# Kernel tuning notes

Measured on AMD Instinct MI355X. Metric: run time of the kernel, lower is better.

Reference implementation:

```python
import jax, jax.numpy as jnp
import numpy as np
from jax import lax

IMAGE_SIZE = 1280
STRIDE = 32
FMP = IMAGE_SIZE // STRIDE          # 40
BPC = 5                             # boxes per cell (5 anchors)
NUM_CLASSES = 80
NMS_THRESH = 0.5
CONF_THRESH = 0.3
N_BOX = FMP * FMP * BPC             # 8000 candidates
ANCHOR_SIZE = np.array([[17, 25], [55, 75], [92, 206], [202, 21], [289, 311]], dtype=np.float32)


def _make_anchors():
    # generate_anchors: per-cell (x,y) grid repeated for each of BPC anchors, tiled anchor wh
    ys, xs = jnp.meshgrid(jnp.arange(FMP, dtype=jnp.float32), jnp.arange(FMP, dtype=jnp.float32), indexing='ij')
    xy = jnp.stack([xs, ys], axis=-1).reshape(-1, 1, 2)                       # [HW,1,2]
    anchor_xy = jnp.broadcast_to(xy, (FMP * FMP, BPC, 2)).reshape(-1, 2)      # [N,2]
    anchor_wh = jnp.broadcast_to(jnp.asarray(ANCHOR_SIZE)[None], (FMP * FMP, BPC, 2)).reshape(-1, 2)
    return jnp.concatenate([anchor_xy, anchor_wh], axis=-1)                   # [N,4]


def setup_inputs() -> dict:
    key = jax.random.key(0)
    k = jax.random.split(key, 5)
    return {
        'cls_feat': jax.random.normal(k[0], (1, 512, FMP, FMP), jnp.float32),
        'reg_feat': jax.random.normal(k[1], (1, 512, FMP, FMP), jnp.float32),
        'w_obj': jax.random.normal(k[2], (BPC, 512), jnp.float32) * 0.02,
        'b_obj': jnp.zeros((BPC,), jnp.float32),
        'w_cls': jax.random.normal(k[3], (NUM_CLASSES * BPC, 512), jnp.float32) * 0.02,
        'b_cls': jnp.zeros((NUM_CLASSES * BPC,), jnp.float32),
        'w_reg': jax.random.normal(k[4], (4 * BPC, 512), jnp.float32) * 0.02,
        'b_reg': jnp.zeros((4 * BPC,), jnp.float32),
    }


def reference(cls_feat, reg_feat, w_obj, b_obj, w_cls, b_cls, w_reg, b_reg):
    # 1x1 convs as channel contractions, already permuted to NHWC like permute(0,2,3,1)
    obj = (jnp.einsum('bchw,oc->bhwo', reg_feat, w_obj) + b_obj).reshape(-1, 1)            # [N,1]
    cls = (jnp.einsum('bchw,oc->bhwo', cls_feat, w_cls) + b_cls).reshape(-1, NUM_CLASSES)  # [N,C]
    reg = (jnp.einsum('bchw,oc->bhwo', reg_feat, w_reg) + b_reg).reshape(-1, 4)            # [N,4]

    scores = jnp.sqrt(jax.nn.sigmoid(obj) * jax.nn.sigmoid(cls))                           # [N,C]

    # decode_boxes
    anchors = _make_anchors()
    ctr = (jax.nn.sigmoid(reg[:, :2]) + anchors[:, :2]) * STRIDE
    wh = jnp.exp(reg[:, 2:]) * anchors[:, 2:]
    bboxes = jnp.concatenate([ctr - wh * 0.5, ctr + wh * 0.5], axis=-1)                    # [N,4] x1y1x2y2

    # postprocess: per-box best class + confidence filter
    labels = jnp.argmax(scores, axis=1)
    score = jnp.take_along_axis(scores, labels[:, None], axis=1)[:, 0]
    valid = score >= CONF_THRESH

    # faithful to original nms(): it re-interprets decoded x1y1x2y2 as cxcywh before IoU
    b2 = jnp.concatenate([bboxes[:, :2] - bboxes[:, 2:] * 0.5,
                          bboxes[:, :2] + bboxes[:, 2:] * 0.5], axis=-1)

    # greedy per-class NMS == global greedy with cross-class IoU gated to 0
    order = jnp.argsort(-score)
    bs = b2[order]
    ls = labels[order]
    vs = valid[order]
    areas = (bs[:, 2] - bs[:, 0]) * (bs[:, 3] - bs[:, 1])
    xx1 = jnp.maximum(bs[:, None, 0], bs[None, :, 0])
    yy1 = jnp.maximum(bs[:, None, 1], bs[None, :, 1])
    xx2 = jnp.minimum(bs[:, None, 2], bs[None, :, 2])
    yy2 = jnp.minimum(bs[:, None, 3], bs[None, :, 3])
    inter = jnp.maximum(1e-10, xx2 - xx1) * jnp.maximum(1e-10, yy2 - yy1)
    iou = inter / (areas[:, None] + areas[None, :] - inter + 1e-14)                        # [N,N]
    same = ls[:, None] == ls[None, :]

    idx = jnp.arange(N_BOX)

    def body(k, supp):
        active = vs[k] & jnp.logical_not(supp[k])
        row = active & (iou[k] > NMS_THRESH) & same[k] & (idx > k)
        return supp | row

    supp = lax.fori_loop(0, N_BOX, body, jnp.zeros(N_BOX, bool))
    keep = jnp.zeros(N_BOX, bool).at[order].set(vs & jnp.logical_not(supp))

    # fixed-size masked outputs (original returns variable-length filtered arrays)
    return bboxes, score, labels, keep
```

## Files before the change

kernel.cpp:

```cpp
#include <hip/hip_runtime.h>
#include <math.h>

#define FMPX 40
#define NPOS 1600
#define NCLS 80
#define NBOX 8000
#define KDIM 512
#define CAP  256

__constant__ float c_aw[5] = {17.f, 55.f, 92.f, 202.f, 289.f};
__constant__ float c_ah[5] = {25.f, 75.f, 206.f, 21.f, 311.f};

__device__ __forceinline__ float sigf(float x) { return 1.0f / (1.0f + expf(-x)); }

__global__ __launch_bounds__(256) void k_gemm(
    const float* __restrict__ cls_feat, const float* __restrict__ reg_feat,
    const float* __restrict__ w_obj, const float* __restrict__ b_obj,
    const float* __restrict__ w_cls, const float* __restrict__ b_cls,
    const float* __restrict__ w_reg, const float* __restrict__ b_reg,
    float* __restrict__ clsRaw,
    float* __restrict__ roRaw)
{
    __shared__ float Ws[16 * KDIM];
    const int mTile = blockIdx.x;
    const int nTile = blockIdx.y;
    const int hw0   = mTile * 64;
    const bool isCls = (nTile < 25);
    const float* feat = isCls ? cls_feat : reg_feat;

    const int pos = threadIdx.x & 63;
    const int og  = threadIdx.x >> 6;

    const float* ap = feat + hw0 + pos;

    float A0[8], A1[8];
#pragma unroll
    for (int t = 0; t < 8; t++) A0[t] = ap[t * NPOS];
#pragma unroll
    for (int t = 0; t < 8; t++) A1[t] = ap[(8 + t) * NPOS];

    for (int i = threadIdx.x * 4; i < 16 * KDIM; i += 256 * 4) {
        int r = i >> 9, k = i & 511;
        const float* src;
        bool valid = true;
        if (isCls) {
            src = w_cls + (nTile * 16 + r) * KDIM + k;
        } else {
            int o = (nTile - 25) * 16 + r;
            if (o < 5)       src = w_obj + o * KDIM + k;
            else if (o < 25) src = w_reg + (o - 5) * KDIM + k;
            else           { src = w_obj; valid = false; }
        }
        float4 v = valid ? *(const float4*)src : make_float4(0.f, 0.f, 0.f, 0.f);
        *(float4*)&Ws[i] = v;
    }

    float bias[4];
    bool ok[4];
#pragma unroll
    for (int j = 0; j < 4; j++) {
        int r = og * 4 + j;
        if (isCls) {
            bias[j] = b_cls[nTile * 16 + r]; ok[j] = true;
        } else {
            int o = (nTile - 25) * 16 + r;
            if (o < 5)       { bias[j] = b_obj[o];     ok[j] = true; }
            else if (o < 25) { bias[j] = b_reg[o - 5]; ok[j] = true; }
            else             { bias[j] = 0.0f;         ok[j] = false; }
        }
    }

    __syncthreads();

    float acc[4] = {0.f, 0.f, 0.f, 0.f};
    const float* wsBase = &Ws[(og * 4) * KDIM];

    for (int kk = 0; kk < KDIM - 16; kk += 16) {
#pragma unroll
        for (int j = 0; j < 4; j++) {
            const float* wp = wsBase + j * KDIM + kk;
            acc[j] += A0[0] * wp[0]; acc[j] += A0[1] * wp[1];
            acc[j] += A0[2] * wp[2]; acc[j] += A0[3] * wp[3];
            acc[j] += A0[4] * wp[4]; acc[j] += A0[5] * wp[5];
            acc[j] += A0[6] * wp[6]; acc[j] += A0[7] * wp[7];
        }
#pragma unroll
        for (int t = 0; t < 8; t++) A0[t] = ap[(kk + 16 + t) * NPOS];
#pragma unroll
        for (int j = 0; j < 4; j++) {
            const float* wp = wsBase + j * KDIM + kk + 8;
            acc[j] += A1[0] * wp[0]; acc[j] += A1[1] * wp[1];
            acc[j] += A1[2] * wp[2]; acc[j] += A1[3] * wp[3];
            acc[j] += A1[4] * wp[4]; acc[j] += A1[5] * wp[5];
            acc[j] += A1[6] * wp[6]; acc[j] += A1[7] * wp[7];
        }
#pragma unroll
        for (int t = 0; t < 8; t++) A1[t] = ap[(kk + 24 + t) * NPOS];
    }
    {
        const int kk = KDIM - 16;
#pragma unroll
        for (int j = 0; j < 4; j++) {
            const float* wp = wsBase + j * KDIM + kk;
            acc[j] += A0[0] * wp[0]; acc[j] += A0[1] * wp[1];
            acc[j] += A0[2] * wp[2]; acc[j] += A0[3] * wp[3];
            acc[j] += A0[4] * wp[4]; acc[j] += A0[5] * wp[5];
            acc[j] += A0[6] * wp[6]; acc[j] += A0[7] * wp[7];
        }
#pragma unroll
        for (int j = 0; j < 4; j++) {
            const float* wp = wsBase + j * KDIM + kk + 8;
            acc[j] += A1[0] * wp[0]; acc[j] += A1[1] * wp[1];
            acc[j] += A1[2] * wp[2]; acc[j] += A1[3] * wp[3];
            acc[j] += A1[4] * wp[4]; acc[j] += A1[5] * wp[5];
            acc[j] += A1[6] * wp[6]; acc[j] += A1[7] * wp[7];
        }
    }

    const int hw = hw0 + pos;
    if (isCls) {
        float4 rv = make_float4(acc[0] + bias[0], acc[1] + bias[1],
                                acc[2] + bias[2], acc[3] + bias[3]);
        *(float4*)&clsRaw[hw * 400 + nTile * 16 + og * 4] = rv;
    } else {
#pragma unroll
        for (int j = 0; j < 4; j++) {
            int o = (nTile - 25) * 16 + og * 4 + j;
            if (ok[j]) roRaw[hw * 25 + o] = acc[j] + bias[j];
        }
    }
}

__global__ __launch_bounds__(256) void k_box(
    const float* __restrict__ clsRaw, const float* __restrict__ roRaw,
    float* __restrict__ out,
    float4* __restrict__ nmsBox, float* __restrict__ nmsArea,
    float2* __restrict__ sl)
{
    const int n = blockIdx.x * 4 + (threadIdx.x >> 6);
    const int lane = threadIdx.x & 63;
    const int hw = n / 5, a = n % 5;

    const float sobj = sigf(roRaw[hw * 25 + a]);
    const float* cbase = clsRaw + hw * 400 + a * 80;

    const int l4 = (lane < 20) ? lane : 19;
    float4 cs = *(const float4*)(cbase + l4 * 4);

    float s0 = sqrtf(sobj * sigf(cs.x));
    float s1 = sqrtf(sobj * sigf(cs.y));
    float s2 = sqrtf(sobj * sigf(cs.z));
    float s3 = sqrtf(sobj * sigf(cs.w));
    float v = s0; int bi = l4 * 4;
    if (s1 > v) { v = s1; bi = l4 * 4 + 1; }
    if (s2 > v) { v = s2; bi = l4 * 4 + 2; }
    if (s3 > v) { v = s3; bi = l4 * 4 + 3; }
    if (lane >= 20) { v = -1.0f; bi = 0x7FFFFFFF; }

#pragma unroll
    for (int off = 32; off >= 1; off >>= 1) {
        float ov = __shfl_xor(v, off);
        int   oi = __shfl_xor(bi, off);
        if (ov > v || (ov == v && oi < bi)) { v = ov; bi = oi; }
    }

    if (lane == 0) {
        const float* rp = roRaw + hw * 25 + 5 + a * 4;
        float r0 = rp[0], r1 = rp[1], r2 = rp[2], r3 = rp[3];
        float gx = (float)(hw % FMPX), gy = (float)(hw / FMPX);
        float cx = (sigf(r0) + gx) * 32.0f;
        float cy = (sigf(r1) + gy) * 32.0f;
        float wv = expf(r2) * c_aw[a];
        float hv = expf(r3) * c_ah[a];
        float x1 = cx - wv * 0.5f, y1 = cy - hv * 0.5f;
        float x2 = cx + wv * 0.5f, y2 = cy + hv * 0.5f;

        out[n * 4 + 0] = x1; out[n * 4 + 1] = y1;
        out[n * 4 + 2] = x2; out[n * 4 + 3] = y2;
        out[32000 + n] = v;
        out[40000 + n] = (float)bi;
        out[48000 + n] = 0.0f;
        sl[n] = make_float2(v, (float)bi);

        float nx1 = x1 - x2 * 0.5f, ny1 = y1 - y2 * 0.5f;
        float nx2 = x1 + x2 * 0.5f, ny2 = y1 + y2 * 0.5f;
        nmsBox[n]  = make_float4(nx1, ny1, nx2, ny2);
        nmsArea[n] = (nx2 - nx1) * (ny2 - ny1);
    }
}

__global__ __launch_bounds__(256) void k_nms(
    const float2* __restrict__ sl,
    const float4* __restrict__ nmsBox, const float* __restrict__ nmsArea,
    float* __restrict__ keepOut)
{
    const int c = blockIdx.x;

    __shared__ float ss[CAP];
    __shared__ int   si[CAP];
    __shared__ float bx1[CAP], by1[CAP], bx2[CAP], by2[CAP], bar[CAP];
    __shared__ int   supp[CAP];
    __shared__ int   cnt;

    if (threadIdx.x == 0) cnt = 0;
    __syncthreads();

    for (int i = threadIdx.x; i < NBOX; i += 256) {
        float2 p = sl[i];
        if (p.x >= 0.3f && (int)p.y == c) {
            int q = atomicAdd(&cnt, 1);
            if (q < CAP) { ss[q] = p.x; si[q] = i; }
        }
    }
    __syncthreads();

    int m = cnt;
    if (m > CAP) m = CAP;

    int P = 2;
    while (P < m) P <<= 1;
    for (int i = threadIdx.x; i < P; i += 256) {
        if (i >= m) { ss[i] = -INFINITY; si[i] = 0x7FFFFFFF; }
    }
    __syncthreads();

    for (int size = 2; size <= P; size <<= 1) {
        for (int stride = size >> 1; stride > 0; stride >>= 1) {
            for (int t = threadIdx.x; t < P / 2; t += 256) {
                int lo = 2 * stride * (t / stride) + (t % stride);
                int hi = lo + stride;
                bool desc = ((lo & size) == 0);
                float slo = ss[lo], shi = ss[hi];
                int   ilo = si[lo], ihi = si[hi];
                bool loBetter = (slo > shi) || (slo == shi && ilo < ihi);
                bool doSwap = desc ? !loBetter : loBetter;
                if (doSwap) { ss[lo] = shi; ss[hi] = slo; si[lo] = ihi; si[hi] = ilo; }
            }
            __syncthreads();
        }
    }

    for (int i = threadIdx.x; i < m; i += 256) {
        int n = si[i];
        float4 b = nmsBox[n];
        bx1[i] = b.x; by1[i] = b.y; bx2[i] = b.z; by2[i] = b.w;
        bar[i] = nmsArea[n];
        supp[i] = 0;
    }
    __syncthreads();

    for (int k = 0; k < m; k++) {
        if (!supp[k]) {
            float kx1 = bx1[k], ky1 = by1[k], kx2 = bx2[k], ky2 = by2[k], ka = bar[k];
            for (int j = k + 1 + threadIdx.x; j < m; j += 256) {
                float xx1 = fmaxf(kx1, bx1[j]);
                float yy1 = fmaxf(ky1, by1[j]);
                float xx2 = fminf(kx2, bx2[j]);
                float yy2 = fminf(ky2, by2[j]);
                float inter = fmaxf(1e-10f, xx2 - xx1) * fmaxf(1e-10f, yy2 - yy1);
                float iou = inter / ((ka + bar[j] - inter) + 1e-14f);
                if (iou > 0.5f) supp[j] = 1;
            }
        }
        __syncthreads();
    }

    for (int j = threadIdx.x; j < m; j += 256) {
        if (!supp[j]) keepOut[si[j]] = 1.0f;
    }
}

extern "C" void kernel_launch(void* const* d_in, const int* in_sizes, int n_in,
                              void* d_out, int out_size, void* d_ws, size_t ws_size,
                              hipStream_t stream) {
    const float* cls_feat = (const float*)d_in[0];
    const float* reg_feat = (const float*)d_in[1];
    const float* w_obj    = (const float*)d_in[2];
    const float* b_obj    = (const float*)d_in[3];
    const float* w_cls    = (const float*)d_in[4];
    const float* b_cls    = (const float*)d_in[5];
    const float* w_reg    = (const float*)d_in[6];
    const float* b_reg    = (const float*)d_in[7];

    float* out = (float*)d_out;
    float* ws  = (float*)d_ws;

    float*  clsRaw    = ws;
    float*  roRaw     = ws + 640000;
    float4* nmsBox    = (float4*)(ws + 680000);
    float*  nmsArea   = ws + 712000;
    float2* sl        = (float2*)(ws + 720000);

    k_gemm<<<dim3(25, 27), 256, 0, stream>>>(cls_feat, reg_feat,
                                             w_obj, b_obj, w_cls, b_cls, w_reg, b_reg,
                                             clsRaw, roRaw);
    k_box<<<NBOX / 4, 256, 0, stream>>>(clsRaw, roRaw, out, nmsBox, nmsArea, sl);
    k_nms<<<NCLS, 256, 0, stream>>>(sl, nmsBox, nmsArea, out + 48000);
}
```

Before: 149.5 us.

## Use wave-uniform scalar weight loads in GEMM and single-wave register NMS

The GEMM no longer stages the 16x512 weight tile in shared memory. Each wavefront reads its four weight rows straight from global memory through a wave-uniform pointer (readfirstlane), so the compiler can issue scalar loads, and the staging pass and barrier go away. The per-class NMS now runs on a single 64-lane wavefront. Candidate boxes live in registers, and suppression bits and the pivot box are passed by shuffles, which replaces a __syncthreads per candidate. The cost is more global and scalar-cache traffic in the GEMM and fewer threads per NMS block.

```diff
diff --git a/kernel.cpp b/kernel.cpp
--- a/kernel.cpp
+++ b/kernel.cpp
@@ -21,7 +21,6 @@
     float* __restrict__ clsRaw,
     float* __restrict__ roRaw)
 {
-    __shared__ float Ws[16 * KDIM];
     const int mTile = blockIdx.x;
     const int nTile = blockIdx.y;
     const int hw0   = mTile * 64;
@@ -29,56 +28,38 @@
     const float* feat = isCls ? cls_feat : reg_feat;
 
     const int pos = threadIdx.x & 63;
-    const int og  = threadIdx.x >> 6;
-
-    const float* ap = feat + hw0 + pos;
-
-    float A0[8], A1[8];
-#pragma unroll
-    for (int t = 0; t < 8; t++) A0[t] = ap[t * NPOS];
-#pragma unroll
-    for (int t = 0; t < 8; t++) A1[t] = ap[(8 + t) * NPOS];
-
-    for (int i = threadIdx.x * 4; i < 16 * KDIM; i += 256 * 4) {
-        int r = i >> 9, k = i & 511;
-        const float* src;
-        bool valid = true;
-        if (isCls) {
-            src = w_cls + (nTile * 16 + r) * KDIM + k;
-        } else {
-            int o = (nTile - 25) * 16 + r;
-            if (o < 5)       src = w_obj + o * KDIM + k;
-            else if (o < 25) src = w_reg + (o - 5) * KDIM + k;
-            else           { src = w_obj; valid = false; }
-        }
-        float4 v = valid ? *(const float4*)src : make_float4(0.f, 0.f, 0.f, 0.f);
-        *(float4*)&Ws[i] = v;
-    }
-
+    const int og = __builtin_amdgcn_readfirstlane(threadIdx.x >> 6);
+
+    const float* wrow[4];
     float bias[4];
     bool ok[4];
 #pragma unroll
     for (int j = 0; j < 4; j++) {
-        int r = og * 4 + j;
         if (isCls) {
-            bias[j] = b_cls[nTile * 16 + r]; ok[j] = true;
+            int o = nTile * 16 + og * 4 + j;
+            wrow[j] = w_cls + o * KDIM; bias[j] = b_cls[o]; ok[j] = true;
         } else {
-            int o = (nTile - 25) * 16 + r;
-            if (o < 5)       { bias[j] = b_obj[o];     ok[j] = true; }
-            else if (o < 25) { bias[j] = b_reg[o - 5]; ok[j] = true; }
-            else             { bias[j] = 0.0f;         ok[j] = false; }
-        }
-    }
-
-    __syncthreads();
+            int o = (nTile - 25) * 16 + og * 4 + j;
+            if (o < 5)       { wrow[j] = w_obj + o * KDIM;       bias[j] = b_obj[o];     ok[j] = true; }
+            else if (o < 25) { wrow[j] = w_reg + (o - 5) * KDIM; bias[j] = b_reg[o - 5]; ok[j] = true; }
+            else             { wrow[j] = w_obj;                  bias[j] = 0.0f;         ok[j] = false; }
+        }
+    }
+
+    const float* ap = feat + hw0 + pos;
+
+    float A0[8], A1[8];
+#pragma unroll
+    for (int t = 0; t < 8; t++) A0[t] = ap[t * NPOS];
+#pragma unroll
+    for (int t = 0; t < 8; t++) A1[t] = ap[(8 + t) * NPOS];
 
     float acc[4] = {0.f, 0.f, 0.f, 0.f};
-    const float* wsBase = &Ws[(og * 4) * KDIM];
 
     for (int kk = 0; kk < KDIM - 16; kk += 16) {
 #pragma unroll
         for (int j = 0; j < 4; j++) {
-            const float* wp = wsBase + j * KDIM + kk;
+            const float* wp = wrow[j] + kk;
             acc[j] += A0[0] * wp[0]; acc[j] += A0[1] * wp[1];
             acc[j] += A0[2] * wp[2]; acc[j] += A0[3] * wp[3];
             acc[j] += A0[4] * wp[4]; acc[j] += A0[5] * wp[5];
@@ -88,7 +69,7 @@
         for (int t = 0; t < 8; t++) A0[t] = ap[(kk + 16 + t) * NPOS];
 #pragma unroll
         for (int j = 0; j < 4; j++) {
-            const float* wp = wsBase + j * KDIM + kk + 8;
+            const float* wp = wrow[j] + kk + 8;
             acc[j] += A1[0] * wp[0]; acc[j] += A1[1] * wp[1];
             acc[j] += A1[2] * wp[2]; acc[j] += A1[3] * wp[3];
             acc[j] += A1[4] * wp[4]; acc[j] += A1[5] * wp[5];
@@ -101,7 +82,7 @@
         const int kk = KDIM - 16;
 #pragma unroll
         for (int j = 0; j < 4; j++) {
-            const float* wp = wsBase + j * KDIM + kk;
+            const float* wp = wrow[j] + kk;
             acc[j] += A0[0] * wp[0]; acc[j] += A0[1] * wp[1];
             acc[j] += A0[2] * wp[2]; acc[j] += A0[3] * wp[3];
             acc[j] += A0[4] * wp[4]; acc[j] += A0[5] * wp[5];
@@ -109,7 +90,7 @@
         }
 #pragma unroll
         for (int j = 0; j < 4; j++) {
-            const float* wp = wsBase + j * KDIM + kk + 8;
+            const float* wp = wrow[j] + kk + 8;
             acc[j] += A1[0] * wp[0]; acc[j] += A1[1] * wp[1];
             acc[j] += A1[2] * wp[2]; acc[j] += A1[3] * wp[3];
             acc[j] += A1[4] * wp[4]; acc[j] += A1[5] * wp[5];
@@ -189,27 +170,31 @@
     }
 }
 
-__global__ __launch_bounds__(256) void k_nms(
+__global__ __launch_bounds__(64) void k_nms(
     const float2* __restrict__ sl,
     const float4* __restrict__ nmsBox, const float* __restrict__ nmsArea,
     float* __restrict__ keepOut)
 {
     const int c = blockIdx.x;
+    const int lane = threadIdx.x;
 
     __shared__ float ss[CAP];
     __shared__ int   si[CAP];
-    __shared__ float bx1[CAP], by1[CAP], bx2[CAP], by2[CAP], bar[CAP];
-    __shared__ int   supp[CAP];
     __shared__ int   cnt;
 
-    if (threadIdx.x == 0) cnt = 0;
+    if (lane == 0) cnt = 0;
     __syncthreads();
 
-    for (int i = threadIdx.x; i < NBOX; i += 256) {
-        float2 p = sl[i];
+    const float4* sl4 = (const float4*)sl;
+    for (int q = lane; q < NBOX / 2; q += 64) {
+        float4 p = sl4[q];
         if (p.x >= 0.3f && (int)p.y == c) {
-            int q = atomicAdd(&cnt, 1);
-            if (q < CAP) { ss[q] = p.x; si[q] = i; }
+            int t = atomicAdd(&cnt, 1);
+            if (t < CAP) { ss[t] = p.x; si[t] = 2 * q; }
+        }
+        if (p.z >= 0.3f && (int)p.w == c) {
+            int t = atomicAdd(&cnt, 1);
+            if (t < CAP) { ss[t] = p.z; si[t] = 2 * q + 1; }
         }
     }
     __syncthreads();
@@ -219,14 +204,14 @@
 
     int P = 2;
     while (P < m) P <<= 1;
-    for (int i = threadIdx.x; i < P; i += 256) {
+    for (int i = lane; i < P; i += 64) {
         if (i >= m) { ss[i] = -INFINITY; si[i] = 0x7FFFFFFF; }
     }
     __syncthreads();
 
     for (int size = 2; size <= P; size <<= 1) {
         for (int stride = size >> 1; stride > 0; stride >>= 1) {
-            for (int t = threadIdx.x; t < P / 2; t += 256) {
+            for (int t = lane; t < P / 2; t += 64) {
                 int lo = 2 * stride * (t / stride) + (t % stride);
                 int hi = lo + stride;
                 bool desc = ((lo & size) == 0);
@@ -240,33 +225,60 @@
         }
     }
 
-    for (int i = threadIdx.x; i < m; i += 256) {
-        int n = si[i];
-        float4 b = nmsBox[n];
-        bx1[i] = b.x; by1[i] = b.y; bx2[i] = b.z; by2[i] = b.w;
-        bar[i] = nmsArea[n];
-        supp[i] = 0;
-    }
-    __syncthreads();
-
+    float cx1[4], cy1[4], cx2[4], cy2[4], car[4];
+    int   cidx[4];
+    bool  cval[4];
+#pragma unroll
+    for (int s = 0; s < 4; s++) {
+        int j = s * 64 + lane;
+        cval[s] = (j < m);
+        cidx[s] = 0;
+        cx1[s] = 0.f; cy1[s] = 0.f; cx2[s] = 0.f; cy2[s] = 0.f; car[s] = 0.f;
+        if (cval[s]) {
+            int n = si[j];
+            cidx[s] = n;
+            float4 b = nmsBox[n];
+            cx1[s] = b.x; cy1[s] = b.y; cx2[s] = b.z; cy2[s] = b.w;
+            car[s] = nmsArea[n];
+        }
+    }
+
+    int sp = 0;
     for (int k = 0; k < m; k++) {
-        if (!supp[k]) {
-            float kx1 = bx1[k], ky1 = by1[k], kx2 = bx2[k], ky2 = by2[k], ka = bar[k];
-            for (int j = k + 1 + threadIdx.x; j < m; j += 256) {
-                float xx1 = fmaxf(kx1, bx1[j]);
-                float yy1 = fmaxf(ky1, by1[j]);
-                float xx2 = fminf(kx2, bx2[j]);
-                float yy2 = fminf(ky2, by2[j]);
+        const int owner = k & 63, slot = k >> 6;
+        int pk = __shfl(sp, owner);
+        if ((pk >> slot) & 1) continue;
+
+        float vx1 = (slot == 0) ? cx1[0] : (slot == 1) ? cx1[1] : (slot == 2) ? cx1[2] : cx1[3];
+        float vy1 = (slot == 0) ? cy1[0] : (slot == 1) ? cy1[1] : (slot == 2) ? cy1[2] : cy1[3];
+        float vx2 = (slot == 0) ? cx2[0] : (slot == 1) ? cx2[1] : (slot == 2) ? cx2[2] : cx2[3];
+        float vy2 = (slot == 0) ? cy2[0] : (slot == 1) ? cy2[1] : (slot == 2) ? cy2[2] : cy2[3];
+        float var = (slot == 0) ? car[0] : (slot == 1) ? car[1] : (slot == 2) ? car[2] : car[3];
+        float px1 = __shfl(vx1, owner);
+        float py1 = __shfl(vy1, owner);
+        float px2 = __shfl(vx2, owner);
+        float py2 = __shfl(vy2, owner);
+        float pa  = __shfl(var, owner);
+
+#pragma unroll
+        for (int s = 0; s < 4; s++) {
+            if (s * 64 + 63 <= k) continue;
+            int j = s * 64 + lane;
+            if (j > k && j < m) {
+                float xx1 = fmaxf(px1, cx1[s]);
+                float yy1 = fmaxf(py1, cy1[s]);
+                float xx2 = fminf(px2, cx2[s]);
+                float yy2 = fminf(py2, cy2[s]);
                 float inter = fmaxf(1e-10f, xx2 - xx1) * fmaxf(1e-10f, yy2 - yy1);
-                float iou = inter / ((ka + bar[j] - inter) + 1e-14f);
-                if (iou > 0.5f) supp[j] = 1;
+                float iou = inter / ((pa + car[s] - inter) + 1e-14f);
+                if (iou > 0.5f) sp |= (1 << s);
             }
         }
-        __syncthreads();
-    }
-
-    for (int j = threadIdx.x; j < m; j += 256) {
-        if (!supp[j]) keepOut[si[j]] = 1.0f;
+    }
+
+#pragma unroll
+    for (int s = 0; s < 4; s++) {
+        if (cval[s] && !((sp >> s) & 1)) keepOut[cidx[s]] = 1.0f;
     }
 }
 
@@ -295,5 +307,5 @@
                                              w_obj, b_obj, w_cls, b_cls, w_reg, b_reg,
                                              clsRaw, roRaw);
     k_box<<<NBOX / 4, 256, 0, stream>>>(clsRaw, roRaw, out, nmsBox, nmsArea, sl);
-    k_nms<<<NCLS, 256, 0, stream>>>(sl, nmsBox, nmsArea, out + 48000);
+    k_nms<<<NCLS, 64, 0, stream>>>(sl, nmsBox, nmsArea, out + 48000);
 }
```

Measured after the change: 218.9 us. +46.5%, slower.
